# Optimization experiments

Measured on AMD Instinct MI355X. Metric: run time of the kernel, lower is better.

Reference implementation:

```python
import jax, jax.numpy as jnp
import numpy as np

B, T, D, H = 4, 2048, 512, 8
DH = D // H

def setup_inputs() -> dict:
    key = jax.random.key(0)
    k1, k2, k3, k4 = jax.random.split(key, 4)
    scale = 1.0 / np.sqrt(D)
    return {
        "x": jax.random.normal(k1, (B, T, D), dtype=jnp.float32),
        "attn_mask": jnp.ones((B, T), dtype=jnp.int32),
        "bias": jax.random.normal(k2, (B, T, T), dtype=jnp.float32),
        "W_qkv": jax.random.normal(k3, (D, 3 * D), dtype=jnp.float32) * scale,
        "W_out": jax.random.normal(k4, (D, D), dtype=jnp.float32) * scale,
    }

def reference(x, attn_mask, bias, W_qkv, W_out):
    qkv = x @ W_qkv                      # [B,T,3D]
    q, k, v = jnp.split(qkv, 3, axis=-1)
    def heads(t):                        # [B,T,D] -> [B,H,T,DH]
        return t.reshape(B, T, H, DH).transpose(0, 2, 1, 3)
    q, k, v = heads(q), heads(k), heads(v)
    logits = jnp.einsum('bhqd,bhkd->bhqk', q, k) / np.sqrt(DH)
    logits = logits + bias[:, None, :, :]
    mask = (attn_mask[:, None, None, :] != 0)
    logits = jnp.where(mask, logits, -jnp.inf)
    attn = jax.nn.softmax(logits, axis=-1)
    out = jnp.einsum('bhqk,bhkd->bhqd', attn, v)  # [B,H,T,DH]
    out = out.transpose(0, 2, 1, 3).reshape(B, T, D)
    return out @ W_out
```

## Files before the change

### kernel.cpp

```cpp
#include <hip/hip_runtime.h>
#include <hip/hip_bf16.h>
#include <stdint.h>

#define Bc 4
#define Tc 2048
#define Dc 512
#define Hc 8

typedef __bf16 bf16x8 __attribute__((ext_vector_type(8)));
typedef float  f32x4  __attribute__((ext_vector_type(4)));
typedef unsigned short u16x8 __attribute__((ext_vector_type(8)));

__device__ __forceinline__ unsigned short f2b(float f) {
  union { float f; unsigned u; } v; v.f = f;
  unsigned r = v.u + 0x7fffu + ((v.u >> 16) & 1u);
  return (unsigned short)(r >> 16);
}

__device__ __forceinline__ bf16x8 ld_frag(const unsigned short* p) {
  u16x8 u = *(const u16x8*)p;
  return __builtin_bit_cast(bf16x8, u);
}

__device__ __forceinline__ void gload_lds16(const unsigned short* g, unsigned short* l) {
  __builtin_amdgcn_global_load_lds((const __attribute__((address_space(1))) void*)g,
                                   (__attribute__((address_space(3))) void*)l,
                                   16, 0, 0);
}

__global__ __launch_bounds__(256) void cvt_bf16(const float* __restrict__ in,
                                                unsigned short* __restrict__ out, int n) {
  int i = (blockIdx.x * 256 + threadIdx.x) * 8;
  if (i >= n) return;
  float4 a = *(const float4*)&in[i];
  float4 b = *(const float4*)&in[i + 4];
  u16x8 r;
  r[0] = f2b(a.x); r[1] = f2b(a.y); r[2] = f2b(a.z); r[3] = f2b(a.w);
  r[4] = f2b(b.x); r[5] = f2b(b.y); r[6] = f2b(b.z); r[7] = f2b(b.w);
  *(u16x8*)&out[i] = r;
}

__global__ __launch_bounds__(256) void transp_bf16(const float* __restrict__ in,
                                                   unsigned short* __restrict__ out,
                                                   int R, int C) {
  __shared__ float tile[32][33];
  int c0 = blockIdx.x * 32, r0 = blockIdx.y * 32;
  int lx = threadIdx.x & 31, ly = threadIdx.x >> 5;
  #pragma unroll
  for (int i = 0; i < 32; i += 8) tile[ly + i][lx] = in[(size_t)(r0 + ly + i) * C + c0 + lx];
  __syncthreads();
  #pragma unroll
  for (int i = 0; i < 32; i += 8) out[(size_t)(c0 + ly + i) * R + r0 + lx] = f2b(tile[lx][ly + i]);
}

__global__ __launch_bounds__(256) void transp_v(const unsigned short* __restrict__ qkv,
                                                unsigned short* __restrict__ vtg) {
  __shared__ unsigned short tile[32][34];
  int t0 = blockIdx.x * 32;
  int d0 = blockIdx.y * 32;
  int b  = blockIdx.z;
  int lx = threadIdx.x & 31, ly = threadIdx.x >> 5;
  #pragma unroll
  for (int i = 0; i < 32; i += 8)
    tile[ly + i][lx] = qkv[(size_t)(b * Tc + t0 + ly + i) * 1536 + 1024 + d0 + lx];
  __syncthreads();
  #pragma unroll
  for (int i = 0; i < 32; i += 8)
    vtg[(size_t)(b * 512 + d0 + ly + i) * Tc + t0 + lx] = tile[lx][ly + i];
}

template <int N, int OUTF32>
__global__ __launch_bounds__(256) void gemm_bt(const unsigned short* __restrict__ A,
                                               const unsigned short* __restrict__ Bt,
                                               void* __restrict__ Cout, int M, int K) {
  __shared__ unsigned short As[128 * 32];
  __shared__ unsigned short Bs[128 * 32];
  const int tid = threadIdx.x;
  const int lane = tid & 63;
  const int wid = tid >> 6;
  const int wm = (wid >> 1) * 64;
  const int wn = (wid & 1) * 64;
  const int m0 = blockIdx.x * 128;
  const int n0 = blockIdx.y * 128;
  const int l15 = lane & 15;
  const int lg = lane >> 4;

  f32x4 acc[4][4];
  #pragma unroll
  for (int i = 0; i < 4; i++)
    #pragma unroll
    for (int j = 0; j < 4; j++) acc[i][j] = (f32x4){0.f, 0.f, 0.f, 0.f};

  const int srow = tid >> 2;
  const int scol = (tid & 3) * 8;

  for (int k0 = 0; k0 < K; k0 += 32) {
    __syncthreads();
    gload_lds16(&A[(size_t)(m0 + srow) * K + k0 + scol],      &As[tid * 8]);
    gload_lds16(&A[(size_t)(m0 + 64 + srow) * K + k0 + scol], &As[2048 + tid * 8]);
    gload_lds16(&Bt[(size_t)(n0 + srow) * K + k0 + scol],      &Bs[tid * 8]);
    gload_lds16(&Bt[(size_t)(n0 + 64 + srow) * K + k0 + scol], &Bs[2048 + tid * 8]);
    __syncthreads();
    bf16x8 af[4], bfr[4];
    #pragma unroll
    for (int m = 0; m < 4; m++) af[m] = ld_frag(&As[(wm + m * 16 + l15) * 32 + lg * 8]);
    #pragma unroll
    for (int n = 0; n < 4; n++) bfr[n] = ld_frag(&Bs[(wn + n * 16 + l15) * 32 + lg * 8]);
    #pragma unroll
    for (int m = 0; m < 4; m++)
      #pragma unroll
      for (int n = 0; n < 4; n++)
        acc[m][n] = __builtin_amdgcn_mfma_f32_16x16x32_bf16(af[m], bfr[n], acc[m][n], 0, 0, 0);
  }

  #pragma unroll
  for (int m = 0; m < 4; m++)
    #pragma unroll
    for (int n = 0; n < 4; n++)
      #pragma unroll
      for (int j = 0; j < 4; j++) {
        int row = m0 + wm + m * 16 + lg * 4 + j;
        int col = n0 + wn + n * 16 + l15;
        float v = acc[m][n][j];
        if (OUTF32) ((float*)Cout)[(size_t)row * N + col] = v;
        else ((unsigned short*)Cout)[(size_t)row * N + col] = f2b(v);
      }
}

__global__ __launch_bounds__(256) void attn_kernel(const unsigned short* __restrict__ qkv,
                                                   const unsigned short* __restrict__ vtg,
                                                   const float* __restrict__ bias,
                                                   const int* __restrict__ amask,
                                                   unsigned short* __restrict__ ctx) {
  __shared__ unsigned short Ks[64 * 64];
  __shared__ unsigned short Vs[64 * 64];
  __shared__ unsigned short Pl[4][16 * 64];

  const int NQ = Tc / 64;
  const int bid = blockIdx.x;
  const int b = bid / (Hc * NQ);
  const int h = (bid / NQ) % Hc;
  const int q0 = (bid % NQ) * 64;
  const int tid = threadIdx.x;
  const int lane = tid & 63;
  const int w = tid >> 6;
  const int l15 = lane & 15;
  const int lg = lane >> 4;

  const int qrow = q0 + w * 16 + l15;
  const size_t qoff = (size_t)(b * Tc + qrow) * 1536 + h * 64;
  bf16x8 qf0 = ld_frag(&qkv[qoff + lg * 8]);
  bf16x8 qf1 = ld_frag(&qkv[qoff + 32 + lg * 8]);

  u16x8 ou;
  #pragma unroll
  for (int e = 0; e < 8; e++) ou[e] = 0x3f80;
  const bf16x8 ones = __builtin_bit_cast(bf16x8, ou);

  f32x4 o[4];
  f32x4 osum = (f32x4){0.f, 0.f, 0.f, 0.f};
  #pragma unroll
  for (int n = 0; n < 4; n++) o[n] = (f32x4){0.f, 0.f, 0.f, 0.f};

  const int skey = tid >> 3;
  const int sc = tid & 7;
  const int sgc = sc ^ (skey & 7);

  const size_t kcol = (size_t)b * Tc * 1536 + 512 + h * 64;
  const unsigned short* vrow = &vtg[(size_t)(b * 512 + h * 64) * Tc];

  const float* bp[4];
  #pragma unroll
  for (int j = 0; j < 4; j++)
    bp[j] = bias + (size_t)(b * Tc + q0 + w * 16 + lg * 4 + j) * Tc + l15;
  const int* mp = amask + b * Tc + l15;

  for (int kt = 0; kt < Tc; kt += 64) {
    __syncthreads();
    {
      const size_t kbase = kcol + (size_t)kt * 1536;
      gload_lds16(&qkv[kbase + (size_t)skey * 1536 + sgc * 8],        &Ks[tid * 8]);
      gload_lds16(&qkv[kbase + (size_t)(skey + 32) * 1536 + sgc * 8], &Ks[2048 + tid * 8]);
      gload_lds16(&vrow[(size_t)skey * Tc + kt + sgc * 8],        &Vs[tid * 8]);
      gload_lds16(&vrow[(size_t)(skey + 32) * Tc + kt + sgc * 8], &Vs[2048 + tid * 8]);
    }
    float bv[4][4];
    #pragma unroll
    for (int j = 0; j < 4; j++)
      #pragma unroll
      for (int t2 = 0; t2 < 4; t2++) bv[t2][j] = bp[j][kt + t2 * 16];
    float madd[4];
    #pragma unroll
    for (int t2 = 0; t2 < 4; t2++) madd[t2] = mp[kt + t2 * 16] ? 0.f : -1e30f;
    __syncthreads();

    f32x4 s[4];
    #pragma unroll
    for (int t2 = 0; t2 < 4; t2++) {
      int key = t2 * 16 + l15;
      bf16x8 kb0 = ld_frag(&Ks[key * 64 + ((lg) ^ (key & 7)) * 8]);
      bf16x8 kb1 = ld_frag(&Ks[key * 64 + ((4 + lg) ^ (key & 7)) * 8]);
      f32x4 z = (f32x4){0.f, 0.f, 0.f, 0.f};
      z = __builtin_amdgcn_mfma_f32_16x16x32_bf16(qf0, kb0, z, 0, 0, 0);
      z = __builtin_amdgcn_mfma_f32_16x16x32_bf16(qf1, kb1, z, 0, 0, 0);
      s[t2] = z;
    }

    #pragma unroll
    for (int t2 = 0; t2 < 4; t2++)
      #pragma unroll
      for (int j = 0; j < 4; j++) {
        float val = fmaf(s[t2][j], 0.125f, bv[t2][j]) + madd[t2];
        s[t2][j] = __expf(val);
      }

    #pragma unroll
    for (int t2 = 0; t2 < 4; t2++)
      #pragma unroll
      for (int j = 0; j < 4; j++) {
        int r = lg * 4 + j;
        int c = t2 * 2 + (l15 >> 3);
        int cp = c ^ (r & 7);
        Pl[w][r * 64 + cp * 8 + (l15 & 7)] = f2b(s[t2][j]);
      }

    #pragma unroll
    for (int ks = 0; ks < 2; ks++) {
      bf16x8 pa = ld_frag(&Pl[w][l15 * 64 + ((ks * 4 + lg) ^ (l15 & 7)) * 8]);
      osum = __builtin_amdgcn_mfma_f32_16x16x32_bf16(pa, ones, osum, 0, 0, 0);
      #pragma unroll
      for (int n = 0; n < 4; n++) {
        int d = n * 16 + l15;
        bf16x8 vb = ld_frag(&Vs[d * 64 + ((ks * 4 + lg) ^ (d & 7)) * 8]);
        o[n] = __builtin_amdgcn_mfma_f32_16x16x32_bf16(pa, vb, o[n], 0, 0, 0);
      }
    }
  }

  #pragma unroll
  for (int n = 0; n < 4; n++)
    #pragma unroll
    for (int j = 0; j < 4; j++) {
      int q = q0 + w * 16 + lg * 4 + j;
      ctx[(size_t)(b * Tc + q) * Dc + h * 64 + n * 16 + l15] = f2b(o[n][j] / osum[j]);
    }
}

extern "C" void kernel_launch(void* const* d_in, const int* in_sizes, int n_in,
                              void* d_out, int out_size, void* d_ws, size_t ws_size,
                              hipStream_t stream) {
  const float* x     = (const float*)d_in[0];
  const int*   amask = (const int*)d_in[1];
  const float* bias  = (const float*)d_in[2];
  const float* Wqkv  = (const float*)d_in[3];
  const float* Wout  = (const float*)d_in[4];
  float* out = (float*)d_out;
  char* ws = (char*)d_ws;

  unsigned short* xb    = (unsigned short*)(ws + 0);
  unsigned short* wqkvT = (unsigned short*)(ws + 8388608);
  unsigned short* woutT = (unsigned short*)(ws + 9961472);
  unsigned short* qkv   = (unsigned short*)(ws + 10485760);
  unsigned short* ctx   = (unsigned short*)(ws + 35651584);
  unsigned short* vtg   = (unsigned short*)(ws + 44040192);

  cvt_bf16<<<2048, 256, 0, stream>>>(x, xb, Bc * Tc * Dc);
  transp_bf16<<<dim3(48, 16), 256, 0, stream>>>(Wqkv, wqkvT, 512, 1536);
  transp_bf16<<<dim3(16, 16), 256, 0, stream>>>(Wout, woutT, 512, 512);
  gemm_bt<1536, 0><<<dim3(64, 12), 256, 0, stream>>>(xb, wqkvT, (void*)qkv, 8192, 512);
  transp_v<<<dim3(64, 16, 4), 256, 0, stream>>>(qkv, vtg);
  attn_kernel<<<1024, 256, 0, stream>>>(qkv, vtg, bias, amask, ctx);
  gemm_bt<512, 1><<<dim3(64, 4), 256, 0, stream>>>(ctx, woutT, (void*)out, 8192, 512);
}
```

Baseline: 152.6 us.

## Double-buffer K/V tiles in LDS and prefetch bias/mask one tile ahead

The attention loop now keeps two LDS buffers for the K and V tiles. It issues the async global-to-LDS loads for the next key tile before computing on the current one, and drops one of the two barriers per iteration. The bias and mask values for the next tile are also loaded into registers during the current tile's softmax and PV phase, to hide the latency of the bias stream. The software bf16 rounding of P is replaced with the native conversion. This costs double the K/V LDS footprint and more live registers, which may reduce occupancy.

```diff
diff --git a/kernel.cpp b/kernel.cpp
--- a/kernel.cpp
+++ b/kernel.cpp
@@ -15,6 +15,11 @@
   union { float f; unsigned u; } v; v.f = f;
   unsigned r = v.u + 0x7fffu + ((v.u >> 16) & 1u);
   return (unsigned short)(r >> 16);
+}
+
+__device__ __forceinline__ unsigned short f2b_native(float f) {
+  __bf16 b = (__bf16)f;
+  return __builtin_bit_cast(unsigned short, b);
 }
 
 __device__ __forceinline__ bf16x8 ld_frag(const unsigned short* p) {
@@ -132,8 +137,8 @@
                                                    const float* __restrict__ bias,
                                                    const int* __restrict__ amask,
                                                    unsigned short* __restrict__ ctx) {
-  __shared__ unsigned short Ks[64 * 64];
-  __shared__ unsigned short Vs[64 * 64];
+  __shared__ unsigned short Ks[2][64 * 64];
+  __shared__ unsigned short Vs[2][64 * 64];
   __shared__ unsigned short Pl[4][16 * 64];
 
   const int NQ = Tc / 64;
@@ -175,31 +180,45 @@
     bp[j] = bias + (size_t)(b * Tc + q0 + w * 16 + lg * 4 + j) * Tc + l15;
   const int* mp = amask + b * Tc + l15;
 
+  {
+    const size_t kbase = kcol;
+    gload_lds16(&qkv[kbase + (size_t)skey * 1536 + sgc * 8],        &Ks[0][tid * 8]);
+    gload_lds16(&qkv[kbase + (size_t)(skey + 32) * 1536 + sgc * 8], &Ks[0][2048 + tid * 8]);
+    gload_lds16(&vrow[(size_t)skey * Tc + sgc * 8],        &Vs[0][tid * 8]);
+    gload_lds16(&vrow[(size_t)(skey + 32) * Tc + sgc * 8], &Vs[0][2048 + tid * 8]);
+  }
+  float bv[4][4];
+  float madd[4];
+  #pragma unroll
+  for (int j = 0; j < 4; j++)
+    #pragma unroll
+    for (int t2 = 0; t2 < 4; t2++) bv[t2][j] = bp[j][t2 * 16];
+  #pragma unroll
+  for (int t2 = 0; t2 < 4; t2++) madd[t2] = mp[t2 * 16] ? 0.f : -1e30f;
+  __syncthreads();
+
+  int cur = 0;
   for (int kt = 0; kt < Tc; kt += 64) {
-    __syncthreads();
-    {
-      const size_t kbase = kcol + (size_t)kt * 1536;
-      gload_lds16(&qkv[kbase + (size_t)skey * 1536 + sgc * 8],        &Ks[tid * 8]);
-      gload_lds16(&qkv[kbase + (size_t)(skey + 32) * 1536 + sgc * 8], &Ks[2048 + tid * 8]);
-      gload_lds16(&vrow[(size_t)skey * Tc + kt + sgc * 8],        &Vs[tid * 8]);
-      gload_lds16(&vrow[(size_t)(skey + 32) * Tc + kt + sgc * 8], &Vs[2048 + tid * 8]);
-    }
-    float bv[4][4];
-    #pragma unroll
-    for (int j = 0; j < 4; j++)
-      #pragma unroll
-      for (int t2 = 0; t2 < 4; t2++) bv[t2][j] = bp[j][kt + t2 * 16];
-    float madd[4];
-    #pragma unroll
-    for (int t2 = 0; t2 < 4; t2++) madd[t2] = mp[kt + t2 * 16] ? 0.f : -1e30f;
-    __syncthreads();
+    if (kt + 64 < Tc) {
+      const int nkt = kt + 64;
+      const size_t kbase = kcol + (size_t)nkt * 1536;
+      unsigned short* ksb = &Ks[cur ^ 1][0];
+      unsigned short* vsb = &Vs[cur ^ 1][0];
+      gload_lds16(&qkv[kbase + (size_t)skey * 1536 + sgc * 8],        &ksb[tid * 8]);
+      gload_lds16(&qkv[kbase + (size_t)(skey + 32) * 1536 + sgc * 8], &ksb[2048 + tid * 8]);
+      gload_lds16(&vrow[(size_t)skey * Tc + nkt + sgc * 8],        &vsb[tid * 8]);
+      gload_lds16(&vrow[(size_t)(skey + 32) * Tc + nkt + sgc * 8], &vsb[2048 + tid * 8]);
+    }
+
+    const unsigned short* ksc = &Ks[cur][0];
+    const unsigned short* vsc = &Vs[cur][0];
 
     f32x4 s[4];
     #pragma unroll
     for (int t2 = 0; t2 < 4; t2++) {
       int key = t2 * 16 + l15;
-      bf16x8 kb0 = ld_frag(&Ks[key * 64 + ((lg) ^ (key & 7)) * 8]);
-      bf16x8 kb1 = ld_frag(&Ks[key * 64 + ((4 + lg) ^ (key & 7)) * 8]);
+      bf16x8 kb0 = ld_frag(&ksc[key * 64 + ((lg) ^ (key & 7)) * 8]);
+      bf16x8 kb1 = ld_frag(&ksc[key * 64 + ((4 + lg) ^ (key & 7)) * 8]);
       f32x4 z = (f32x4){0.f, 0.f, 0.f, 0.f};
       z = __builtin_amdgcn_mfma_f32_16x16x32_bf16(qf0, kb0, z, 0, 0, 0);
       z = __builtin_amdgcn_mfma_f32_16x16x32_bf16(qf1, kb1, z, 0, 0, 0);
@@ -214,6 +233,16 @@
         s[t2][j] = __expf(val);
       }
 
+    if (kt + 64 < Tc) {
+      const int nkt = kt + 64;
+      #pragma unroll
+      for (int j = 0; j < 4; j++)
+        #pragma unroll
+        for (int t2 = 0; t2 < 4; t2++) bv[t2][j] = bp[j][nkt + t2 * 16];
+      #pragma unroll
+      for (int t2 = 0; t2 < 4; t2++) madd[t2] = mp[nkt + t2 * 16] ? 0.f : -1e30f;
+    }
+
     #pragma unroll
     for (int t2 = 0; t2 < 4; t2++)
       #pragma unroll
@@ -221,7 +250,7 @@
         int r = lg * 4 + j;
         int c = t2 * 2 + (l15 >> 3);
         int cp = c ^ (r & 7);
-        Pl[w][r * 64 + cp * 8 + (l15 & 7)] = f2b(s[t2][j]);
+        Pl[w][r * 64 + cp * 8 + (l15 & 7)] = f2b_native(s[t2][j]);
       }
 
     #pragma unroll
@@ -231,10 +260,13 @@
       #pragma unroll
       for (int n = 0; n < 4; n++) {
         int d = n * 16 + l15;
-        bf16x8 vb = ld_frag(&Vs[d * 64 + ((ks * 4 + lg) ^ (d & 7)) * 8]);
+        bf16x8 vb = ld_frag(&vsc[d * 64 + ((ks * 4 + lg) ^ (d & 7)) * 8]);
         o[n] = __builtin_amdgcn_mfma_f32_16x16x32_bf16(pa, vb, o[n], 0, 0, 0);
       }
     }
+
+    __syncthreads();
+    cur ^= 1;
   }
 
   #pragma unroll
```

Result: slower. 166.4 us (+9.0%).

## Transpose score MFMA for vectorized bias loads and padded P tile

Applied to the files above, without the earlier changes.

Swaps the MFMA operands in the QK^T product so each lane holds four consecutive keys for a single query row. That lets bias and mask be read as float4/int4 vectors instead of scalar strided loads, and P can be written to LDS as ushort4 into a 72-stride padded tile instead of a swizzled scalar layout. It also folds the exponent into exp2 with a pre-scaled bias, switches to native bf16 conversion, and sets launch bounds to 5 waves per SIMD. The risks are register pressure from the occupancy hint and LDS bank conflicts in the padded layout.

```diff
diff --git a/kernel.cpp b/kernel.cpp
--- a/kernel.cpp
+++ b/kernel.cpp
@@ -15,6 +15,11 @@
   union { float f; unsigned u; } v; v.f = f;
   unsigned r = v.u + 0x7fffu + ((v.u >> 16) & 1u);
   return (unsigned short)(r >> 16);
+}
+
+__device__ __forceinline__ unsigned short f2b_native(float f) {
+  __bf16 b = (__bf16)f;
+  return __builtin_bit_cast(unsigned short, b);
 }
 
 __device__ __forceinline__ bf16x8 ld_frag(const unsigned short* p) {
@@ -127,14 +132,14 @@
       }
 }
 
-__global__ __launch_bounds__(256) void attn_kernel(const unsigned short* __restrict__ qkv,
-                                                   const unsigned short* __restrict__ vtg,
-                                                   const float* __restrict__ bias,
-                                                   const int* __restrict__ amask,
-                                                   unsigned short* __restrict__ ctx) {
+__global__ __launch_bounds__(256, 5) void attn_kernel(const unsigned short* __restrict__ qkv,
+                                                      const unsigned short* __restrict__ vtg,
+                                                      const float* __restrict__ bias,
+                                                      const int* __restrict__ amask,
+                                                      unsigned short* __restrict__ ctx) {
   __shared__ unsigned short Ks[64 * 64];
   __shared__ unsigned short Vs[64 * 64];
-  __shared__ unsigned short Pl[4][16 * 64];
+  __shared__ unsigned short Pt[4][16 * 72];
 
   const int NQ = Tc / 64;
   const int bid = blockIdx.x;
@@ -147,6 +152,8 @@
   const int l15 = lane & 15;
   const int lg = lane >> 4;
 
+  const float LOG2E = 1.44269504f;
+
   const int qrow = q0 + w * 16 + l15;
   const size_t qoff = (size_t)(b * Tc + qrow) * 1536 + h * 64;
   bf16x8 qf0 = ld_frag(&qkv[qoff + lg * 8]);
@@ -169,11 +176,10 @@
   const size_t kcol = (size_t)b * Tc * 1536 + 512 + h * 64;
   const unsigned short* vrow = &vtg[(size_t)(b * 512 + h * 64) * Tc];
 
-  const float* bp[4];
-  #pragma unroll
-  for (int j = 0; j < 4; j++)
-    bp[j] = bias + (size_t)(b * Tc + q0 + w * 16 + lg * 4 + j) * Tc + l15;
-  const int* mp = amask + b * Tc + l15;
+  const float* bq = bias + (size_t)(b * Tc + q0 + w * 16 + l15) * Tc;
+  const int* mq = amask + b * Tc;
+
+  unsigned short* ptw = &Pt[w][0];
 
   for (int kt = 0; kt < Tc; kt += 64) {
     __syncthreads();
@@ -184,14 +190,16 @@
       gload_lds16(&vrow[(size_t)skey * Tc + kt + sgc * 8],        &Vs[tid * 8]);
       gload_lds16(&vrow[(size_t)(skey + 32) * Tc + kt + sgc * 8], &Vs[2048 + tid * 8]);
     }
-    float bv[4][4];
-    #pragma unroll
-    for (int j = 0; j < 4; j++)
-      #pragma unroll
-      for (int t2 = 0; t2 < 4; t2++) bv[t2][j] = bp[j][kt + t2 * 16];
-    float madd[4];
-    #pragma unroll
-    for (int t2 = 0; t2 < 4; t2++) madd[t2] = mp[kt + t2 * 16] ? 0.f : -1e30f;
+    float bf_[4][4];
+    #pragma unroll
+    for (int t2 = 0; t2 < 4; t2++) {
+      float4 bb = *(const float4*)&bq[kt + t2 * 16 + lg * 4];
+      int4 mm = *(const int4*)&mq[kt + t2 * 16 + lg * 4];
+      bf_[t2][0] = mm.x ? bb.x * LOG2E : -1e30f;
+      bf_[t2][1] = mm.y ? bb.y * LOG2E : -1e30f;
+      bf_[t2][2] = mm.z ? bb.z * LOG2E : -1e30f;
+      bf_[t2][3] = mm.w ? bb.w * LOG2E : -1e30f;
+    }
     __syncthreads();
 
     f32x4 s[4];
@@ -201,32 +209,30 @@
       bf16x8 kb0 = ld_frag(&Ks[key * 64 + ((lg) ^ (key & 7)) * 8]);
       bf16x8 kb1 = ld_frag(&Ks[key * 64 + ((4 + lg) ^ (key & 7)) * 8]);
       f32x4 z = (f32x4){0.f, 0.f, 0.f, 0.f};
-      z = __builtin_amdgcn_mfma_f32_16x16x32_bf16(qf0, kb0, z, 0, 0, 0);
-      z = __builtin_amdgcn_mfma_f32_16x16x32_bf16(qf1, kb1, z, 0, 0, 0);
+      z = __builtin_amdgcn_mfma_f32_16x16x32_bf16(kb0, qf0, z, 0, 0, 0);
+      z = __builtin_amdgcn_mfma_f32_16x16x32_bf16(kb1, qf1, z, 0, 0, 0);
       s[t2] = z;
     }
 
     #pragma unroll
     for (int t2 = 0; t2 < 4; t2++)
       #pragma unroll
-      for (int j = 0; j < 4; j++) {
-        float val = fmaf(s[t2][j], 0.125f, bv[t2][j]) + madd[t2];
-        s[t2][j] = __expf(val);
-      }
-
-    #pragma unroll
-    for (int t2 = 0; t2 < 4; t2++)
-      #pragma unroll
-      for (int j = 0; j < 4; j++) {
-        int r = lg * 4 + j;
-        int c = t2 * 2 + (l15 >> 3);
-        int cp = c ^ (r & 7);
-        Pl[w][r * 64 + cp * 8 + (l15 & 7)] = f2b(s[t2][j]);
-      }
+      for (int j = 0; j < 4; j++)
+        s[t2][j] = exp2f(fmaf(s[t2][j], 0.125f * LOG2E, bf_[t2][j]));
+
+    #pragma unroll
+    for (int t2 = 0; t2 < 4; t2++) {
+      ushort4 pw;
+      pw.x = f2b_native(s[t2][0]);
+      pw.y = f2b_native(s[t2][1]);
+      pw.z = f2b_native(s[t2][2]);
+      pw.w = f2b_native(s[t2][3]);
+      *(ushort4*)&ptw[l15 * 72 + t2 * 16 + lg * 4] = pw;
+    }
 
     #pragma unroll
     for (int ks = 0; ks < 2; ks++) {
-      bf16x8 pa = ld_frag(&Pl[w][l15 * 64 + ((ks * 4 + lg) ^ (l15 & 7)) * 8]);
+      bf16x8 pa = ld_frag(&ptw[l15 * 72 + ks * 32 + lg * 8]);
       osum = __builtin_amdgcn_mfma_f32_16x16x32_bf16(pa, ones, osum, 0, 0, 0);
       #pragma unroll
       for (int n = 0; n < 4; n++) {
```

Measured after the change: 158.8 us. 1.04x slower.
